# Performance work log

Measured on AMD Instinct MI355X. Metric: run time of the kernel, lower is better.

The kernel has to match this reference:

```python
import jax, jax.numpy as jnp
import numpy as np

B, N, D_IN, D, H_HEADS, DH, M_LAND, ITERS, NCLS = 2, 16384, 1024, 512, 8, 64, 256, 6, 2


def layer_norm(x, g, b, eps=1e-5):
    mu = x.mean(-1, keepdims=True)
    var = ((x - mu) ** 2).mean(-1, keepdims=True)
    return (x - mu) * jax.lax.rsqrt(var + eps) * g + b


def pinv_iter(x, iters):
    # Moore-Penrose pseudo-inverse via Newton-Schulz style iteration (lucidrains nystrom-attention)
    col = jnp.abs(x).sum(-1)
    row = jnp.abs(x).sum(-2)
    z = jnp.swapaxes(x, -1, -2) / (jnp.max(col) * jnp.max(row))
    I = jnp.eye(x.shape[-1], dtype=x.dtype)
    for _ in range(iters):
        xz = x @ z
        z = 0.25 * z @ (13.0 * I - xz @ (15.0 * I - xz @ (7.0 * I - xz)))
    return z


def depthwise_conv(x, w, pad_h, pad_w):
    # x: [B,C,H,W], w: [C,1,kh,kw], groups=C
    return jax.lax.conv_general_dilated(
        x, w, (1, 1), ((pad_h, pad_h), (pad_w, pad_w)),
        dimension_numbers=('NCHW', 'OIHW', 'NCHW'), feature_group_count=x.shape[1])


def nystrom_attention(x, w_qkv, w_out, b_out, res_w):
    b, n, _ = x.shape
    pad = (-n) % M_LAND
    xp = jnp.pad(x, ((0, 0), (pad, 0), (0, 0)))  # pad at front
    npad = n + pad
    qkv = xp @ w_qkv                              # [b, npad, 3D]
    q, k, v = jnp.split(qkv, 3, axis=-1)
    split_heads = lambda t: t.reshape(b, npad, H_HEADS, DH).transpose(0, 2, 1, 3)
    q = split_heads(q) * (DH ** -0.5)
    k = split_heads(k)
    v = split_heads(v)
    l = npad // M_LAND
    # landmarks: mean over contiguous groups '(m l) d -> m d'
    ql = q.reshape(b, H_HEADS, M_LAND, l, DH).mean(3)
    kl = k.reshape(b, H_HEADS, M_LAND, l, DH).mean(3)
    sim1 = jnp.einsum('bhnd,bhmd->bhnm', q, kl)   # [b,h,npad,m]
    sim2 = jnp.einsum('bhid,bhjd->bhij', ql, kl)  # [b,h,m,m]
    sim3 = jnp.einsum('bhmd,bhnd->bhmn', ql, k)   # [b,h,m,npad]
    a1 = jax.nn.softmax(sim1, -1)
    a2 = jax.nn.softmax(sim2, -1)
    a3 = jax.nn.softmax(sim3, -1)
    a2inv = pinv_iter(a2, ITERS)
    out = (a1 @ a2inv) @ (a3 @ v)                 # [b,h,npad,dh]
    # residual depthwise conv over sequence dim, kernel (33,1), per head
    out = out + depthwise_conv(v, res_w, 16, 0)
    out = out.transpose(0, 2, 1, 3).reshape(b, npad, D)
    out = out @ w_out + b_out                     # dropout is identity in eval
    return out[:, -n:]


def ppeg(x, Hs, Ws, w7, b7, w5, b5, w3, b3):
    Bx, _, C = x.shape
    cls_tok, feat = x[:, :1], x[:, 1:]
    f = feat.transpose(0, 2, 1).reshape(Bx, C, Hs, Ws)
    y = (f
         + depthwise_conv(f, w7, 3, 3) + b7[None, :, None, None]
         + depthwise_conv(f, w5, 2, 2) + b5[None, :, None, None]
         + depthwise_conv(f, w3, 1, 1) + b3[None, :, None, None])
    y = y.reshape(Bx, C, Hs * Ws).transpose(0, 2, 1)
    return jnp.concatenate([cls_tok, y], axis=1)


def _forward(x, w_feat, b_feat, cls_token, ln1_g, ln1_b, qkv1, out1_w, out1_b, res1_w,
             ppeg_w7, ppeg_b7, ppeg_w5, ppeg_b5, ppeg_w3, ppeg_b3,
             ln2_g, ln2_b, qkv2, out2_w, out2_b, res2_w, lnf_g, lnf_b, cls_w, cls_b):
    h = jax.nn.gelu(x @ w_feat + b_feat)          # feature embed (dropout off)
    n = h.shape[1]
    side = int(np.ceil(np.sqrt(n)))
    add = side * side - n
    h = jnp.concatenate([h, h[:, :add]], axis=1)  # pad bag to square
    cls = jnp.broadcast_to(cls_token, (h.shape[0], 1, D))
    h = jnp.concatenate([cls, h], axis=1)
    h = h + nystrom_attention(layer_norm(h, ln1_g, ln1_b), qkv1, out1_w, out1_b, res1_w)
    h = ppeg(h, side, side, ppeg_w7, ppeg_b7, ppeg_w5, ppeg_b5, ppeg_w3, ppeg_b3)
    h = h + nystrom_attention(layer_norm(h, ln2_g, ln2_b), qkv2, out2_w, out2_b, res2_w)
    feat0 = layer_norm(h, lnf_g, lnf_b)[:, 0]
    return feat0 @ cls_w + cls_b                  # logits [B, n_classes]


def setup_inputs() -> dict:
    key = jax.random.key(0)
    ks = jax.random.split(key, 16)
    s = jnp.float32(0.02)
    return {
        'x': jax.random.normal(ks[0], (B, N, D_IN), jnp.float32),
        'w_feat': jax.random.normal(ks[1], (D_IN, D), jnp.float32) * s,
        'b_feat': jnp.zeros((D,), jnp.float32),
        'cls_token': jax.random.normal(ks[2], (1, 1, D), jnp.float32) * jnp.float32(1e-6),
        'ln1_g': jnp.ones((D,), jnp.float32), 'ln1_b': jnp.zeros((D,), jnp.float32),
        'qkv1': jax.random.normal(ks[3], (D, 3 * D), jnp.float32) * s,
        'out1_w': jax.random.normal(ks[4], (D, D), jnp.float32) * s,
        'out1_b': jnp.zeros((D,), jnp.float32),
        'res1_w': jax.random.normal(ks[5], (H_HEADS, 1, 33, 1), jnp.float32) * s,
        'ppeg_w7': jax.random.normal(ks[6], (D, 1, 7, 7), jnp.float32) * s,
        'ppeg_b7': jnp.zeros((D,), jnp.float32),
        'ppeg_w5': jax.random.normal(ks[7], (D, 1, 5, 5), jnp.float32) * s,
        'ppeg_b5': jnp.zeros((D,), jnp.float32),
        'ppeg_w3': jax.random.normal(ks[8], (D, 1, 3, 3), jnp.float32) * s,
        'ppeg_b3': jnp.zeros((D,), jnp.float32),
        'ln2_g': jnp.ones((D,), jnp.float32), 'ln2_b': jnp.zeros((D,), jnp.float32),
        'qkv2': jax.random.normal(ks[9], (D, 3 * D), jnp.float32) * s,
        'out2_w': jax.random.normal(ks[10], (D, D), jnp.float32) * s,
        'out2_b': jnp.zeros((D,), jnp.float32),
        'res2_w': jax.random.normal(ks[11], (H_HEADS, 1, 33, 1), jnp.float32) * s,
        'lnf_g': jnp.ones((D,), jnp.float32), 'lnf_b': jnp.zeros((D,), jnp.float32),
        'cls_w': jax.random.normal(ks[12], (D, NCLS), jnp.float32) * s,
        'cls_b': jnp.zeros((NCLS,), jnp.float32),
    }


def reference(x, w_feat, b_feat, cls_token, ln1_g, ln1_b, qkv1, out1_w, out1_b, res1_w,
              ppeg_w7, ppeg_b7, ppeg_w5, ppeg_b5, ppeg_w3, ppeg_b3,
              ln2_g, ln2_b, qkv2, out2_w, out2_b, res2_w, lnf_g, lnf_b, cls_w, cls_b):
    return _forward(x, w_feat, b_feat, cls_token, ln1_g, ln1_b, qkv1, out1_w, out1_b, res1_w,
                    ppeg_w7, ppeg_b7, ppeg_w5, ppeg_b5, ppeg_w3, ppeg_b3,
                    ln2_g, ln2_b, qkv2, out2_w, out2_b, res2_w, lnf_g, lnf_b, cls_w, cls_b)
```

## Files before the change

### kernel.cpp

```cpp
#include <hip/hip_runtime.h>
#include <cstdint>
#include <cstddef>

#define BB 2
#define TT 16385
#define NPAD 16640
#define DD 512
#define HH 8
#define DHH 64
#define MLAND 256
#define PADF 255
#define A3KC 26
#define A3CH 640

typedef __attribute__((ext_vector_type(8))) _Float16 f16x8;
typedef __attribute__((ext_vector_type(4))) float f32x4;

__device__ __forceinline__ float gelu_f(float v) {
  float c = 0.7978845608028654f * (v + 0.044715f * v * v * v);
  return 0.5f * v * (1.0f + tanhf(c));
}

__device__ __forceinline__ unsigned short f16_1(float a) {
  _Float16 h = (_Float16)a;
  return __builtin_bit_cast(unsigned short, h);
}
__device__ __forceinline__ float f16f(unsigned u) {
  return (float)__builtin_bit_cast(_Float16, (unsigned short)(u & 0xffffu));
}
__device__ __forceinline__ unsigned pk_f16(float a, float b) {
  return (unsigned)f16_1(a) | ((unsigned)f16_1(b) << 16);
}
__device__ __forceinline__ void split2h(float a, float b, unsigned& hi, unsigned& lo) {
  _Float16 ah = (_Float16)a, bh = (_Float16)b;
  hi = (unsigned)__builtin_bit_cast(unsigned short, ah) |
       ((unsigned)__builtin_bit_cast(unsigned short, bh) << 16);
  lo = pk_f16(a - (float)ah, b - (float)bh);
}
__device__ __forceinline__ void store4h(float4 v, unsigned short* dh,
                                        unsigned short* dl) {
  unsigned h0, l0, h1, l1;
  split2h(v.x, v.y, h0, l0);
  split2h(v.z, v.w, h1, l1);
  *(uint2*)dh = make_uint2(h0, h1);
  *(uint2*)dl = make_uint2(l0, l1);
}

__device__ __forceinline__ void gload16(const unsigned short* g, short* l) {
  __builtin_amdgcn_global_load_lds(
      (const __attribute__((address_space(1))) void*)g,
      (__attribute__((address_space(3))) void*)l, 16, 0, 0);
}

__global__ void k_set_cls(float* __restrict__ h, const float* __restrict__ cls) {
  h[(size_t)blockIdx.x * TT * DD + threadIdx.x] = cls[threadIdx.x];
}
__global__ void k_copy_cls(float* __restrict__ dst, const float* __restrict__ src) {
  size_t o = (size_t)blockIdx.x * TT * DD + threadIdx.x;
  dst[o] = src[o];
}

__global__ __launch_bounds__(256) void k_cvt_wt(
    const float* __restrict__ W, unsigned short* __restrict__ Wth, int K, int N) {
  __shared__ float tile[32][33];
  int kb = blockIdx.x * 32, nb = blockIdx.y * 32;
  int t = threadIdx.x;
  int tr = t >> 3, tc4 = (t & 7) * 4;
  float4 v = *(const float4*)(W + (size_t)(kb + tr) * N + nb + tc4);
  tile[tr][tc4 + 0] = v.x;
  tile[tr][tc4 + 1] = v.y;
  tile[tr][tc4 + 2] = v.z;
  tile[tr][tc4 + 3] = v.w;
  __syncthreads();
  int n = nb + tr;
  ushort4 hs;
  hs.x = f16_1(tile[tc4 + 0][tr]);
  hs.y = f16_1(tile[tc4 + 1][tr]);
  hs.z = f16_1(tile[tc4 + 2][tr]);
  hs.w = f16_1(tile[tc4 + 3][tr]);
  *(ushort4*)(Wth + (size_t)n * K + kb + tc4) = hs;
}

template <int MODE>
__global__ __launch_bounds__(512) void k_gemm_mfma(
    const float* __restrict__ A, const unsigned short* __restrict__ Aph,
    const unsigned short* __restrict__ Apl, const unsigned short* __restrict__ Wth,
    const float* __restrict__ bias, void* __restrict__ Cv, int M, int K, int N,
    int lda) {
  __shared__ short Ash[128][44];
  __shared__ short Asl[128][44];
  __shared__ short Bsh[256][44];
  const int t = threadIdx.x;
  int nRow = gridDim.x, nCol = gridDim.y;
  int lin = blockIdx.x + blockIdx.y * nRow;
  int chunk = 8 * nCol;
  int group = lin / chunk;
  int rem = lin - group * chunk;
  int gbase = group * 8;
  int Geff = nRow - gbase;
  if (Geff > 8) Geff = 8;
  const int rb = (gbase + rem % Geff) * 128;
  const int cb = (rem / Geff) * 256;
  const float* Ab = A;
  float* Cf = (float*)Cv;
  unsigned short* Ch = (unsigned short*)Cv;
  if (MODE == 2) {
    int b = blockIdx.z;
    Ab = A + (size_t)b * NPAD * DD + (size_t)PADF * DD;
    Cf = (float*)Cv + (size_t)b * TT * DD;
  }
  const int lane = t & 63, wv = t >> 6;
  const int wr = wv >> 2, wc = wv & 3;
  const int fr = lane & 15, kg = lane >> 4;
  const int srow = t >> 2, skh = (t & 3) * 8;
  const int brow = t >> 1, bkh = (t & 1) * 16;

  f32x4 acc[4][4];
  f32x4 zero4 = {0.f, 0.f, 0.f, 0.f};
#pragma unroll
  for (int i = 0; i < 4; ++i)
#pragma unroll
    for (int j = 0; j < 4; ++j) acc[i][j] = zero4;

  for (int k0 = 0; k0 < K; k0 += 32) {
    __syncthreads();
    if (MODE == 1) {
      const unsigned short* ph = Aph + (size_t)(rb + srow) * lda + k0 + skh;
      const unsigned short* pl = Apl + (size_t)(rb + srow) * lda + k0 + skh;
      *(uint4*)&Ash[srow][skh] = *(const uint4*)ph;
      *(uint4*)&Asl[srow][skh] = *(const uint4*)pl;
    } else {
      int grow = rb + srow;
      float4 f0 = {0, 0, 0, 0}, f1 = {0, 0, 0, 0};
      if (grow < M) {
        const float* p = Ab + (size_t)grow * lda + k0 + skh;
        f0 = *(const float4*)p;
        f1 = *(const float4*)(p + 4);
      }
      unsigned h0, h1, h2, h3, l0, l1, l2, l3;
      split2h(f0.x, f0.y, h0, l0);
      split2h(f0.z, f0.w, h1, l1);
      split2h(f1.x, f1.y, h2, l2);
      split2h(f1.z, f1.w, h3, l3);
      *(uint4*)&Ash[srow][skh] = make_uint4(h0, h1, h2, h3);
      *(uint4*)&Asl[srow][skh] = make_uint4(l0, l1, l2, l3);
    }
    {
      const unsigned short* ph = Wth + (size_t)(cb + brow) * K + k0 + bkh;
      *(uint4*)&Bsh[brow][bkh] = *(const uint4*)ph;
      *(uint4*)&Bsh[brow][bkh + 8] = *(const uint4*)(ph + 8);
    }
    __syncthreads();
    f16x8 ah[4], al[4];
#pragma unroll
    for (int mf = 0; mf < 4; ++mf) {
      ah[mf] = *(const f16x8*)&Ash[wr * 64 + mf * 16 + fr][kg * 8];
      al[mf] = *(const f16x8*)&Asl[wr * 64 + mf * 16 + fr][kg * 8];
    }
#pragma unroll
    for (int nf = 0; nf < 4; ++nf) {
      f16x8 bhf = *(const f16x8*)&Bsh[wc * 64 + nf * 16 + fr][kg * 8];
#pragma unroll
      for (int mf = 0; mf < 4; ++mf) {
        acc[mf][nf] =
            __builtin_amdgcn_mfma_f32_16x16x32_f16(ah[mf], bhf, acc[mf][nf], 0, 0, 0);
        acc[mf][nf] =
            __builtin_amdgcn_mfma_f32_16x16x32_f16(al[mf], bhf, acc[mf][nf], 0, 0, 0);
      }
    }
  }
#pragma unroll
  for (int mf = 0; mf < 4; ++mf) {
#pragma unroll
    for (int r = 0; r < 4; ++r) {
      int row = rb + wr * 64 + mf * 16 + kg * 4 + r;
      if (MODE == 2 && row >= M) continue;
      size_t orow = (MODE == 0) ? (size_t)(row + (row >> 14) + 1) : (size_t)row;
#pragma unroll
      for (int nf = 0; nf < 4; ++nf) {
        int col = cb + wc * 64 + nf * 16 + fr;
        float v = acc[mf][nf][r];
        if (MODE == 0) {
          Cf[orow * DD + col] = gelu_f(v + bias[col]);
        } else if (MODE == 1) {
          Ch[orow * (size_t)N + col] = f16_1(v);
        } else {
          float old = Cf[orow * DD + col];
          Cf[orow * DD + col] = old + v + bias[col];
        }
      }
    }
  }
}

__global__ __launch_bounds__(512) void k_gemm_qkv8(
    const unsigned short* __restrict__ Aph, const unsigned short* __restrict__ Apl,
    const unsigned short* __restrict__ Wth, unsigned short* __restrict__ Ch) {
  __shared__ __align__(16) short Ah[2][128][32];
  __shared__ __align__(16) short Al[2][128][32];
  __shared__ __align__(16) short Bs[2][256][32];
  const int t = threadIdx.x;
  int nRow = gridDim.x, nCol = gridDim.y;
  int lin = blockIdx.x + blockIdx.y * nRow;
  int chunk = 8 * nCol;
  int group = lin / chunk;
  int rem = lin - group * chunk;
  int gbase = group * 8;
  int Geff = nRow - gbase;
  if (Geff > 8) Geff = 8;
  const int rb = (gbase + rem % Geff) * 128;
  const int cb = (rem / Geff) * 256;
  const int lane = t & 63, wv = t >> 6;
  const int wr = wv >> 2, wc = wv & 3;
  const int fr = lane & 15, kg = lane >> 4;
  const int lr4 = lane >> 2;
  const int ss = (lane & 3) ^ (lr4 & 3);

  f32x4 acc[4][4];
  f32x4 zero4 = {0.f, 0.f, 0.f, 0.f};
#pragma unroll
  for (int i = 0; i < 4; ++i)
#pragma unroll
    for (int j = 0; j < 4; ++j) acc[i][j] = zero4;

  auto STAGE = [&](int kt, int bf) {
    const int k0 = kt * 32;
    {
      int lr = wv * 16;
      gload16(Aph + (size_t)(rb + lr + lr4) * DD + k0 + ss * 8, &Ah[bf][lr][0]);
      gload16(Apl + (size_t)(rb + lr + lr4) * DD + k0 + ss * 8, &Al[bf][lr][0]);
    }
#pragma unroll
    for (int j = 0; j < 2; ++j) {
      int lr = wv * 32 + j * 16;
      gload16(Wth + (size_t)(cb + lr + lr4) * DD + k0 + ss * 8, &Bs[bf][lr][0]);
    }
  };

  STAGE(0, 0);
  STAGE(1, 1);
  const int sl = ((kg ^ (fr & 3))) * 8;
  for (int kt = 0; kt < 16; ++kt) {
    if (kt < 15) {
      asm volatile("s_waitcnt vmcnt(4)" ::: "memory");
    } else {
      asm volatile("s_waitcnt vmcnt(0)" ::: "memory");
    }
    __builtin_amdgcn_sched_barrier(0);
    __builtin_amdgcn_s_barrier();
    const int bf = kt & 1;
    f16x8 ah[4], al[4];
#pragma unroll
    for (int mf = 0; mf < 4; ++mf) {
      ah[mf] = *(const f16x8*)&Ah[bf][wr * 64 + mf * 16 + fr][sl];
      al[mf] = *(const f16x8*)&Al[bf][wr * 64 + mf * 16 + fr][sl];
    }
#pragma unroll
    for (int nf = 0; nf < 4; ++nf) {
      f16x8 bhf = *(const f16x8*)&Bs[bf][wc * 64 + nf * 16 + fr][sl];
#pragma unroll
      for (int mf = 0; mf < 4; ++mf) {
        acc[mf][nf] =
            __builtin_amdgcn_mfma_f32_16x16x32_f16(ah[mf], bhf, acc[mf][nf], 0, 0, 0);
        acc[mf][nf] =
            __builtin_amdgcn_mfma_f32_16x16x32_f16(al[mf], bhf, acc[mf][nf], 0, 0, 0);
      }
    }
    __builtin_amdgcn_s_barrier();
    if (kt + 2 < 16) STAGE(kt + 2, bf);
  }
#pragma unroll
  for (int mf = 0; mf < 4; ++mf) {
#pragma unroll
    for (int r = 0; r < 4; ++r) {
      int row = rb + wr * 64 + mf * 16 + kg * 4 + r;
#pragma unroll
      for (int nf = 0; nf < 4; ++nf) {
        int col = cb + wc * 64 + nf * 16 + fr;
        Ch[(size_t)row * 1536 + col] = f16_1(acc[mf][nf][r]);
      }
    }
  }
}

__global__ __launch_bounds__(256) void k_ln_pad(
    unsigned short* __restrict__ xph, unsigned short* __restrict__ xpl,
    const float* __restrict__ h, const float* __restrict__ gam,
    const float* __restrict__ bet) {
  int w = threadIdx.x >> 6, lane = threadIdx.x & 63;
  int row = blockIdx.x * 4 + w;
  if (row >= BB * TT) return;
  int b = row / TT, i = row - b * TT;
  const float* src = h + (size_t)row * DD;
  float4 x0 = *(const float4*)(src + lane * 4);
  float4 x1 = *(const float4*)(src + 256 + lane * 4);
  float s = x0.x + x0.y + x0.z + x0.w + x1.x + x1.y + x1.z + x1.w;
  for (int o = 32; o; o >>= 1) s += __shfl_xor(s, o);
  float mu = s * (1.f / 512.f);
  float q = (x0.x - mu) * (x0.x - mu) + (x0.y - mu) * (x0.y - mu) +
            (x0.z - mu) * (x0.z - mu) + (x0.w - mu) * (x0.w - mu) +
            (x1.x - mu) * (x1.x - mu) + (x1.y - mu) * (x1.y - mu) +
            (x1.z - mu) * (x1.z - mu) + (x1.w - mu) * (x1.w - mu);
  for (int o = 32; o; o >>= 1) q += __shfl_xor(q, o);
  float rs = rsqrtf(q * (1.f / 512.f) + 1e-5f);
  float4 g0 = *(const float4*)(gam + lane * 4);
  float4 g1 = *(const float4*)(gam + 256 + lane * 4);
  float4 b0 = *(const float4*)(bet + lane * 4);
  float4 b1 = *(const float4*)(bet + 256 + lane * 4);
  float4 o0, o1;
  o0.x = (x0.x - mu) * rs * g0.x + b0.x;
  o0.y = (x0.y - mu) * rs * g0.y + b0.y;
  o0.z = (x0.z - mu) * rs * g0.z + b0.z;
  o0.w = (x0.w - mu) * rs * g0.w + b0.w;
  o1.x = (x1.x - mu) * rs * g1.x + b1.x;
  o1.y = (x1.y - mu) * rs * g1.y + b1.y;
  o1.z = (x1.z - mu) * rs * g1.z + b1.z;
  o1.w = (x1.w - mu) * rs * g1.w + b1.w;
  size_t ro = ((size_t)b * NPAD + PADF + i) * DD;
  store4h(o0, xph + ro + lane * 4, xpl + ro + lane * 4);
  store4h(o1, xph + ro + 256 + lane * 4, xpl + ro + 256 + lane * 4);
}

__global__ void k_zero_pad(unsigned short* __restrict__ xph,
                           unsigned short* __restrict__ xpl) {
  int r = blockIdx.x;
  int b = r / PADF, j = r - b * PADF;
  size_t ro = ((size_t)b * NPAD + j) * DD;
  ((unsigned*)(xph + ro))[threadIdx.x] = 0u;
  ((unsigned*)(xpl + ro))[threadIdx.x] = 0u;
}

__global__ __launch_bounds__(256) void k_landmarks(
    float* __restrict__ ql, float* __restrict__ kl,
    const unsigned short* __restrict__ qkv) {
  int t = threadIdx.x;
  int mi = t >> 6, d = t & 63;
  int blk = blockIdx.x;
  int bh = blk >> 6, mg = blk & 63;
  int b = bh >> 3, h = bh & 7;
  int m = mg * 4 + mi;
  const unsigned short* base = qkv + (size_t)b * NPAD * 1536 + h * 64 + d;
  float sq = 0.f, sk = 0.f;
  int t0 = m * 65;
  for (int j = 0; j < 65; ++j) {
    const unsigned short* p = base + (size_t)(t0 + j) * 1536;
    sq += f16f(p[0]);
    sk += f16f(p[512]);
  }
  ql[((size_t)bh * 256 + m) * 64 + d] = sq * (0.125f / 65.f);
  kl[((size_t)bh * 256 + m) * 64 + d] = sk * (1.f / 65.f);
}

__global__ __launch_bounds__(256) void k_sim2(
    float* __restrict__ sim, const float* __restrict__ ql, const float* __restrict__ kl) {
  __shared__ __align__(16) float Aq[64][68];
  __shared__ __align__(16) float Bk[64][68];
  int t = threadIdx.x;
  int tj = blockIdx.x, ti = blockIdx.y, bh = blockIdx.z;
  int r = t >> 2, cc = (t & 3) * 16;
  const float* ap = ql + ((size_t)bh * 256 + ti * 64 + r) * 64 + cc;
  const float* bp = kl + ((size_t)bh * 256 + tj * 64 + r) * 64 + cc;
#pragma unroll
  for (int i = 0; i < 16; i += 4) {
    *(float4*)&Aq[r][cc + i] = *(const float4*)(ap + i);
    *(float4*)&Bk[r][cc + i] = *(const float4*)(bp + i);
  }
  __syncthreads();
  int tx = t & 15, ty = t >> 4;
  float acc[4][4];
#pragma unroll
  for (int i = 0; i < 4; ++i)
#pragma unroll
    for (int j = 0; j < 4; ++j) acc[i][j] = 0.f;
  for (int d = 0; d < 64; d += 4) {
    float4 a4[4], b4[4];
#pragma unroll
    for (int ii = 0; ii < 4; ++ii) a4[ii] = *(float4*)&Aq[ty * 4 + ii][d];
#pragma unroll
    for (int jj = 0; jj < 4; ++jj) b4[jj] = *(float4*)&Bk[tx * 4 + jj][d];
#pragma unroll
    for (int ii = 0; ii < 4; ++ii)
#pragma unroll
      for (int jj = 0; jj < 4; ++jj)
        acc[ii][jj] += a4[ii].x * b4[jj].x + a4[ii].y * b4[jj].y + a4[ii].z * b4[jj].z +
                       a4[ii].w * b4[jj].w;
  }
#pragma unroll
  for (int ii = 0; ii < 4; ++ii)
#pragma unroll
    for (int jj = 0; jj < 4; ++jj)
      sim[((size_t)bh * 256 + ti * 64 + ty * 4 + ii) * 256 + tj * 64 + tx * 4 + jj] =
          acc[ii][jj];
}

__global__ __launch_bounds__(256) void k_softmax256(float* __restrict__ a) {
  int w = threadIdx.x >> 6, lane = threadIdx.x & 63;
  size_t row = (size_t)blockIdx.x * 4 + w;
  float* p = a + row * 256 + lane * 4;
  float4 v = *(float4*)p;
  float m = fmaxf(fmaxf(v.x, v.y), fmaxf(v.z, v.w));
  for (int o = 32; o; o >>= 1) m = fmaxf(m, __shfl_xor(m, o));
  v.x = expf(v.x - m); v.y = expf(v.y - m);
  v.z = expf(v.z - m); v.w = expf(v.w - m);
  float s = v.x + v.y + v.z + v.w;
  for (int o = 32; o; o >>= 1) s += __shfl_xor(s, o);
  float inv = 1.f / s;
  v.x *= inv; v.y *= inv; v.z *= inv; v.w *= inv;
  *(float4*)p = v;
}

__global__ void k_pinv_sums(float* __restrict__ red, const float* __restrict__ a2) {
  int bh = blockIdx.x, t = threadIdx.x;
  const float* Ab = a2 + (size_t)bh * 65536;
  float s = 0.f;
  for (int i = 0; i < 256; ++i) s += fabsf(Ab[(size_t)i * 256 + t]);
  red[bh * 256 + t] = s;
  float c = 0.f;
  const float* rp = Ab + (size_t)t * 256;
  for (int j = 0; j < 256; j += 4) {
    float4 v = *(const float4*)(rp + j);
    c += fabsf(v.x) + fabsf(v.y) + fabsf(v.z) + fabsf(v.w);
  }
  red[4096 + bh * 256 + t] = c;
}

__global__ void k_pinv_scale(float* __restrict__ red) {
  __shared__ float sm[8];
  int t = threadIdx.x;
  float m1 = 0.f, m2 = 0.f;
  for (int k = t; k < 4096; k += 256) {
    m1 = fmaxf(m1, red[k]);
    m2 = fmaxf(m2, red[4096 + k]);
  }
  for (int o = 32; o; o >>= 1) {
    m1 = fmaxf(m1, __shfl_xor(m1, o));
    m2 = fmaxf(m2, __shfl_xor(m2, o));
  }
  int w = t >> 6;
  if ((t & 63) == 0) { sm[w] = m1; sm[4 + w] = m2; }
  __syncthreads();
  if (t == 0) {
    float a = fmaxf(fmaxf(sm[0], sm[1]), fmaxf(sm[2], sm[3]));
    float b = fmaxf(fmaxf(sm[4], sm[5]), fmaxf(sm[6], sm[7]));
    red[8192] = 1.0f / (a * b);
  }
}

__global__ void k_zinit(float* __restrict__ z, const float* __restrict__ a2,
                        const float* __restrict__ red) {
  float s = red[8192];
  int i = blockIdx.x, bh = blockIdx.y, j = threadIdx.x;
  z[((size_t)bh * 256 + i) * 256 + j] = a2[((size_t)bh * 256 + j) * 256 + i] * s;
}

__device__ __forceinline__ void bmm_core(
    short (*Ash)[136], short (*Asl)[136], short (*Bsh)[136], short (*Bsl)[136],
    const float* __restrict__ Ab, const float* __restrict__ Bb, int i0, int j0, int N,
    int t, f32x4 (&acc)[4]) {
  const int lane = t & 63, w = t >> 6;
  const int fr = lane & 15, kg = lane >> 4;
  const int ar = t >> 2, akseg = (t & 3) * 32;
  for (int k0 = 0; k0 < 256; k0 += 128) {
    __syncthreads();
    {
      const float* p = Ab + (size_t)(i0 + ar) * 256 + k0 + akseg;
#pragma unroll
      for (int q = 0; q < 4; ++q) {
        float4 f0 = *(const float4*)(p + q * 8);
        float4 f1 = *(const float4*)(p + q * 8 + 4);
        unsigned h0, h1, h2, h3, l0, l1, l2, l3;
        split2h(f0.x, f0.y, h0, l0);
        split2h(f0.z, f0.w, h1, l1);
        split2h(f1.x, f1.y, h2, l2);
        split2h(f1.z, f1.w, h3, l3);
        *(uint4*)&Ash[ar][akseg + q * 8] = make_uint4(h0, h1, h2, h3);
        *(uint4*)&Asl[ar][akseg + q * 8] = make_uint4(l0, l1, l2, l3);
      }
    }
    {
#pragma unroll
      for (int pass = 0; pass < 8; ++pass) {
        int kr = pass * 16 + (t >> 4);
        int jseg = (t & 15) * 4;
        const float* p = Bb + (size_t)(k0 + kr) * N + j0 + jseg;
        float4 f = *(const float4*)p;
        float fv[4] = {f.x, f.y, f.z, f.w};
#pragma unroll
        for (int c = 0; c < 4; ++c) {
          _Float16 hh = (_Float16)fv[c];
          float lo = fv[c] - (float)hh;
          Bsh[jseg + c][kr] = (short)__builtin_bit_cast(unsigned short, hh);
          Bsl[jseg + c][kr] = (short)f16_1(lo);
        }
      }
    }
    __syncthreads();
#pragma unroll
    for (int kw = 0; kw < 4; ++kw) {
      f16x8 bhf = *(const f16x8*)&Bsh[w * 16 + fr][kw * 32 + kg * 8];
      f16x8 blf = *(const f16x8*)&Bsl[w * 16 + fr][kw * 32 + kg * 8];
#pragma unroll
      for (int mf = 0; mf < 4; ++mf) {
        f16x8 ah = *(const f16x8*)&Ash[mf * 16 + fr][kw * 32 + kg * 8];
        f16x8 al = *(const f16x8*)&Asl[mf * 16 + fr][kw * 32 + kg * 8];
        acc[mf] = __builtin_amdgcn_mfma_f32_16x16x32_f16(ah, bhf, acc[mf], 0, 0, 0);
        acc[mf] = __builtin_amdgcn_mfma_f32_16x16x32_f16(al, bhf, acc[mf], 0, 0, 0);
        acc[mf] = __builtin_amdgcn_mfma_f32_16x16x32_f16(ah, blf, acc[mf], 0, 0, 0);
      }
    }
  }
}

__global__ __launch_bounds__(256) void k_bmm_poly(
    const float* __restrict__ A, const float* __restrict__ Bm,
    const float* __restrict__ E, float* __restrict__ C, float a1, float d1, float e1,
    int N) {
  __shared__ short Ash[64][136];
  __shared__ short Asl[64][136];
  __shared__ short Bsh[64][136];
  __shared__ short Bsl[64][136];
  const int t = threadIdx.x;
  const int bh = blockIdx.z;
  const int i0 = blockIdx.y * 64, j0 = blockIdx.x * 64;
  const int lane = t & 63, w = t >> 6;
  const int fr = lane & 15, kg = lane >> 4;
  f32x4 acc[4];
  f32x4 zero4 = {0.f, 0.f, 0.f, 0.f};
#pragma unroll
  for (int i = 0; i < 4; ++i) acc[i] = zero4;
  bmm_core(Ash, Asl, Bsh, Bsl, A + (size_t)bh * 65536, Bm + (size_t)bh * 256 * N, i0,
           j0, N, t, acc);
  int j = j0 + w * 16 + fr;
#pragma unroll
  for (int mf = 0; mf < 4; ++mf) {
#pragma unroll
    for (int rr = 0; rr < 4; ++rr) {
      int i = i0 + mf * 16 + kg * 4 + rr;
      float v = acc[mf][rr];
      size_t off = (size_t)bh * 256 * N + (size_t)i * N + j;
      float out = a1 * v + ((i == j) ? d1 : 0.f);
      if (E) out += e1 * E[off];
      C[off] = out;
    }
  }
}

__global__ __launch_bounds__(256) void k_bmm_dual(
    const float* __restrict__ A0, const float* __restrict__ A1,
    const float* __restrict__ Bm, float* __restrict__ C0, float* __restrict__ C1,
    float s) {
  __shared__ short Ash[64][136];
  __shared__ short Asl[64][136];
  __shared__ short Bsh[64][136];
  __shared__ short Bsl[64][136];
  const int t = threadIdx.x;
  const int z = blockIdx.z;
  const int bh = z & 15;
  const int sel = z >> 4;
  const float* A = sel ? A1 : A0;
  float* C = sel ? C1 : C0;
  const int i0 = blockIdx.y * 64, j0 = blockIdx.x * 64;
  const int lane = t & 63, w = t >> 6;
  const int fr = lane & 15, kg = lane >> 4;
  f32x4 acc[4];
  f32x4 zero4 = {0.f, 0.f, 0.f, 0.f};
#pragma unroll
  for (int i = 0; i < 4; ++i) acc[i] = zero4;
  bmm_core(Ash, Asl, Bsh, Bsl, A + (size_t)bh * 65536, Bm + (size_t)bh * 65536, i0, j0,
           256, t, acc);
  int j = j0 + w * 16 + fr;
#pragma unroll
  for (int mf = 0; mf < 4; ++mf) {
#pragma unroll
    for (int rr = 0; rr < 4; ++rr) {
      int i = i0 + mf * 16 + kg * 4 + rr;
      size_t off = (size_t)bh * 65536 + (size_t)i * 256 + j;
      C[off] = s * acc[mf][rr];
    }
  }
}

__global__ __launch_bounds__(256, 2) void k_a3v_mfma(
    float* __restrict__ pacc, float* __restrict__ pL,
    const float* __restrict__ ql, const unsigned short* __restrict__ qkv) {
  __shared__ short Ks[64][72];
  __shared__ short Vt[64][72];
  __shared__ short Ps[4][64][72];
  const int t = threadIdx.x;
  const int bh = blockIdx.x;
  const int kc = blockIdx.y;
  const int b = bh >> 3, h = bh & 7;
  const int lane = t & 63, w = t >> 6;
  const int fr = lane & 15, kg = lane >> 4;

  f16x8 qf[4][2];
#pragma unroll
  for (int nf = 0; nf < 4; ++nf) {
    const float* qp = ql + ((size_t)bh * 256 + w * 64 + nf * 16 + fr) * 64 + kg * 8;
#pragma unroll
    for (int kw = 0; kw < 2; ++kw) {
      float4 a = *(const float4*)(qp + kw * 32);
      float4 c = *(const float4*)(qp + kw * 32 + 4);
      uint4 uu = make_uint4(pk_f16(a.x, a.y), pk_f16(a.z, a.w), pk_f16(c.x, c.y),
                            pk_f16(c.z, c.w));
      qf[nf][kw] = *(f16x8*)&uu;
    }
  }
  f32x4 oacc[4][4];
  f32x4 zero4 = {0.f, 0.f, 0.f, 0.f};
#pragma unroll
  for (int i = 0; i < 4; ++i)
#pragma unroll
    for (int j = 0; j < 4; ++j) oacc[i][j] = zero4;
  float Lp[4] = {0.f, 0.f, 0.f, 0.f};

  const int skey = t >> 2, sd = (t & 3) * 16;
  const unsigned short* kbase = qkv + (size_t)b * NPAD * 1536 + 512 + h * 64 + sd;

  for (int it = 0; it < A3CH / 64; ++it) {
    int nt = kc * A3CH + it * 64;
    __syncthreads();
    {
      const unsigned short* kp = kbase + (size_t)(nt + skey) * 1536;
      *(uint4*)&Ks[skey][sd] = *(const uint4*)kp;
      *(uint4*)&Ks[skey][sd + 8] = *(const uint4*)(kp + 8);
      const unsigned short* vp = kp + 512;
      uint4 v01 = *(const uint4*)vp;
      uint4 v23 = *(const uint4*)(vp + 8);
      Vt[sd + 0][skey] = (short)v01.x;
      Vt[sd + 1][skey] = (short)(v01.x >> 16);
      Vt[sd + 2][skey] = (short)v01.y;
      Vt[sd + 3][skey] = (short)(v01.y >> 16);
      Vt[sd + 4][skey] = (short)v01.z;
      Vt[sd + 5][skey] = (short)(v01.z >> 16);
      Vt[sd + 6][skey] = (short)v01.w;
      Vt[sd + 7][skey] = (short)(v01.w >> 16);
      Vt[sd + 8][skey] = (short)v23.x;
      Vt[sd + 9][skey] = (short)(v23.x >> 16);
      Vt[sd + 10][skey] = (short)v23.y;
      Vt[sd + 11][skey] = (short)(v23.y >> 16);
      Vt[sd + 12][skey] = (short)v23.z;
      Vt[sd + 13][skey] = (short)(v23.z >> 16);
      Vt[sd + 14][skey] = (short)v23.w;
      Vt[sd + 15][skey] = (short)(v23.w >> 16);
    }
    __syncthreads();
    f32x4 sacc[4][4];
#pragma unroll
    for (int i = 0; i < 4; ++i)
#pragma unroll
      for (int j = 0; j < 4; ++j) sacc[i][j] = zero4;
#pragma unroll
    for (int kw = 0; kw < 2; ++kw) {
      f16x8 kf[4];
#pragma unroll
      for (int mf = 0; mf < 4; ++mf)
        kf[mf] = *(const f16x8*)&Ks[mf * 16 + fr][kw * 32 + kg * 8];
#pragma unroll
      for (int mf = 0; mf < 4; ++mf)
#pragma unroll
        for (int nf = 0; nf < 4; ++nf)
          sacc[mf][nf] = __builtin_amdgcn_mfma_f32_16x16x32_f16(kf[mf], qf[nf][kw],
                                                                sacc[mf][nf], 0, 0, 0);
    }
#pragma unroll
    for (int mf = 0; mf < 4; ++mf)
#pragma unroll
      for (int nf = 0; nf < 4; ++nf) {
        f32x4 s = sacc[mf][nf];
        float p0 = __expf(s[0]);
        float p1 = __expf(s[1]);
        float p2 = __expf(s[2]);
        float p3 = __expf(s[3]);
        Lp[nf] += (p0 + p1) + (p2 + p3);
        uint2 pw = make_uint2(pk_f16(p0, p1), pk_f16(p2, p3));
        *(uint2*)&Ps[w][nf * 16 + fr][mf * 16 + kg * 4] = pw;
      }
    __syncthreads();
#pragma unroll
    for (int kw = 0; kw < 2; ++kw) {
      f16x8 vf[4], pf[4];
#pragma unroll
      for (int mf = 0; mf < 4; ++mf)
        vf[mf] = *(const f16x8*)&Vt[mf * 16 + fr][kw * 32 + kg * 8];
#pragma unroll
      for (int nf = 0; nf < 4; ++nf)
        pf[nf] = *(const f16x8*)&Ps[w][nf * 16 + fr][kw * 32 + kg * 8];
#pragma unroll
      for (int mf = 0; mf < 4; ++mf)
#pragma unroll
        for (int nf = 0; nf < 4; ++nf)
          oacc[mf][nf] = __builtin_amdgcn_mfma_f32_16x16x32_f16(vf[mf], pf[nf],
                                                                oacc[mf][nf], 0, 0, 0);
    }
  }
  size_t obase = ((size_t)kc * 16 + bh) * 256;
#pragma unroll
  for (int mf = 0; mf < 4; ++mf)
#pragma unroll
    for (int nf = 0; nf < 4; ++nf) {
      int lm = w * 64 + nf * 16 + fr;
      *(f32x4*)(pacc + (obase + lm) * 64 + mf * 16 + kg * 4) = oacc[mf][nf];
    }
#pragma unroll
  for (int nf = 0; nf < 4; ++nf) {
    Lp[nf] += __shfl_xor(Lp[nf], 16);
    Lp[nf] += __shfl_xor(Lp[nf], 32);
  }
  if (lane < 16) {
#pragma unroll
    for (int nf = 0; nf < 4; ++nf)
      pL[obase + w * 64 + nf * 16 + lane] = Lp[nf];
  }
}

__global__ __launch_bounds__(64) void k_a3v_red(
    float* __restrict__ bv, const float* __restrict__ pacc,
    const float* __restrict__ pL) {
  int row = blockIdx.x;
  int d = threadIdx.x;
  float A = 0.f, L = 0.f;
#pragma unroll
  for (int c = 0; c < A3KC; ++c) {
    size_t pr = (size_t)c * 4096 + row;
    A += pacc[pr * 64 + d];
    L += pL[pr];
  }
  bv[(size_t)row * 64 + d] = A / L;
}

__global__ __launch_bounds__(256, 2) void k_att1(
    float* __restrict__ attout, const unsigned short* __restrict__ qkv,
    const float* __restrict__ kl, const float* __restrict__ w2) {
  __shared__ short KLs[64][72];
  __shared__ short W2t[64][72];
  __shared__ short Ps[4][64][72];
  const int t = threadIdx.x;
  const int tile = blockIdx.x, bh = blockIdx.y;
  const int b = bh >> 3, h = bh & 7;
  const int lane = t & 63, w = t >> 6;
  const int fr = lane & 15, kg = lane >> 4;
  const int n0 = tile * 256;

  f16x8 qf[4][2];
#pragma unroll
  for (int nf = 0; nf < 4; ++nf) {
    const unsigned short* qp =
        qkv + ((size_t)b * NPAD + n0 + w * 64 + nf * 16 + fr) * 1536 + h * 64 + kg * 8;
    qf[nf][0] = *(const f16x8*)qp;
    qf[nf][1] = *(const f16x8*)(qp + 32);
  }
  f32x4 oacc[4][4];
  f32x4 zero4 = {0.f, 0.f, 0.f, 0.f};
#pragma unroll
  for (int i = 0; i < 4; ++i)
#pragma unroll
    for (int j = 0; j < 4; ++j) oacc[i][j] = zero4;
  float Lp[4] = {0.f, 0.f, 0.f, 0.f};

  const int sr = t >> 2, sc = (t & 3) * 16;
  for (int cb = 0; cb < 4; ++cb) {
    __syncthreads();
    {
      const float* kp = kl + ((size_t)bh * 256 + cb * 64 + sr) * 64 + sc;
      float4 k0 = *(const float4*)kp;
      float4 k1 = *(const float4*)(kp + 4);
      float4 k2 = *(const float4*)(kp + 8);
      float4 k3 = *(const float4*)(kp + 12);
      *(uint4*)&KLs[sr][sc] =
          make_uint4(pk_f16(k0.x * 0.125f, k0.y * 0.125f),
                     pk_f16(k0.z * 0.125f, k0.w * 0.125f),
                     pk_f16(k1.x * 0.125f, k1.y * 0.125f),
                     pk_f16(k1.z * 0.125f, k1.w * 0.125f));
      *(uint4*)&KLs[sr][sc + 8] =
          make_uint4(pk_f16(k2.x * 0.125f, k2.y * 0.125f),
                     pk_f16(k2.z * 0.125f, k2.w * 0.125f),
                     pk_f16(k3.x * 0.125f, k3.y * 0.125f),
                     pk_f16(k3.z * 0.125f, k3.w * 0.125f));
      const float* wp = w2 + ((size_t)bh * 256 + cb * 64 + sr) * 64 + sc;
      float4 v0 = *(const float4*)wp;
      float4 v1 = *(const float4*)(wp + 4);
      float4 v2 = *(const float4*)(wp + 8);
      float4 v3 = *(const float4*)(wp + 12);
      W2t[sc + 0][sr] = (short)f16_1(v0.x);
      W2t[sc + 1][sr] = (short)f16_1(v0.y);
      W2t[sc + 2][sr] = (short)f16_1(v0.z);
      W2t[sc + 3][sr] = (short)f16_1(v0.w);
      W2t[sc + 4][sr] = (short)f16_1(v1.x);
      W2t[sc + 5][sr] = (short)f16_1(v1.y);
      W2t[sc + 6][sr] = (short)f16_1(v1.z);
      W2t[sc + 7][sr] = (short)f16_1(v1.w);
      W2t[sc + 8][sr] = (short)f16_1(v2.x);
      W2t[sc + 9][sr] = (short)f16_1(v2.y);
      W2t[sc + 10][sr] = (short)f16_1(v2.z);
      W2t[sc + 11][sr] = (short)f16_1(v2.w);
      W2t[sc + 12][sr] = (short)f16_1(v3.x);
      W2t[sc + 13][sr] = (short)f16_1(v3.y);
      W2t[sc + 14][sr] = (short)f16_1(v3.z);
      W2t[sc + 15][sr] = (short)f16_1(v3.w);
    }
    __syncthreads();
    f32x4 sacc[4][4];
#pragma unroll
    for (int i = 0; i < 4; ++i)
#pragma unroll
      for (int j = 0; j < 4; ++j) sacc[i][j] = zero4;
#pragma unroll
    for (int kw = 0; kw < 2; ++kw) {
      f16x8 kf[4];
#pragma unroll
      for (int mf = 0; mf < 4; ++mf)
        kf[mf] = *(const f16x8*)&KLs[mf * 16 + fr][kw * 32 + kg * 8];
#pragma unroll
      for (int mf = 0; mf < 4; ++mf)
#pragma unroll
        for (int nf = 0; nf < 4; ++nf)
          sacc[mf][nf] = __builtin_amdgcn_mfma_f32_16x16x32_f16(kf[mf], qf[nf][kw],
                                                                sacc[mf][nf], 0, 0, 0);
    }
#pragma unroll
    for (int mf = 0; mf < 4; ++mf)
#pragma unroll
      for (int nf = 0; nf < 4; ++nf) {
        f32x4 s = sacc[mf][nf];
        float p0 = __expf(s[0]);
        float p1 = __expf(s[1]);
        float p2 = __expf(s[2]);
        float p3 = __expf(s[3]);
        Lp[nf] += (p0 + p1) + (p2 + p3);
        uint2 pw = make_uint2(pk_f16(p0, p1), pk_f16(p2, p3));
        *(uint2*)&Ps[w][nf * 16 + fr][mf * 16 + kg * 4] = pw;
      }
    __syncthreads();
#pragma unroll
    for (int kw = 0; kw < 2; ++kw) {
      f16x8 vf[4], pf[4];
#pragma unroll
      for (int mf = 0; mf < 4; ++mf)
        vf[mf] = *(const f16x8*)&W2t[mf * 16 + fr][kw * 32 + kg * 8];
#pragma unroll
      for (int nf = 0; nf < 4; ++nf)
        pf[nf] = *(const f16x8*)&Ps[w][nf * 16 + fr][kw * 32 + kg * 8];
#pragma unroll
      for (int mf = 0; mf < 4; ++mf)
#pragma unroll
        for (int nf = 0; nf < 4; ++nf)
          oacc[mf][nf] = __builtin_amdgcn_mfma_f32_16x16x32_f16(vf[mf], pf[nf],
                                                                oacc[mf][nf], 0, 0, 0);
    }
  }
#pragma unroll
  for (int nf = 0; nf < 4; ++nf) {
    Lp[nf] += __shfl_xor(Lp[nf], 16);
    Lp[nf] += __shfl_xor(Lp[nf], 32);
  }
#pragma unroll
  for (int nf = 0; nf < 4; ++nf) {
    float inv = 1.0f / Lp[nf];
    int tok = n0 + w * 64 + nf * 16 + fr;
#pragma unroll
    for (int mf = 0; mf < 4; ++mf) {
      f32x4 o = oacc[mf][nf];
      o[0] *= inv; o[1] *= inv; o[2] *= inv; o[3] *= inv;
      *(f32x4*)(attout + ((size_t)b * NPAD + tok) * DD + h * 64 + mf * 16 + kg * 4) = o;
    }
  }
}

__global__ __launch_bounds__(256) void k_convres(
    float* __restrict__ attout, const unsigned short* __restrict__ qkv,
    const float* __restrict__ resw) {
  __shared__ float vS[96][68];
  __shared__ float w33[33];
  int t = threadIdx.x;
  int tb = blockIdx.x, bh = blockIdx.y;
  int b = bh >> 3, h = bh & 7;
  int n0 = tb * 64;
  if (t < 33) w33[t] = resw[h * 33 + t];
  int sc = (t & 3) * 16;
#pragma unroll
  for (int pass = 0; pass < 2; ++pass) {
    int r = (t >> 2) + pass * 64;
    if (r < 96) {
      int seq = n0 - 16 + r;
      if (seq >= 0 && seq < NPAD) {
        const unsigned short* p =
            qkv + ((size_t)b * NPAD + seq) * 1536 + 1024 + h * 64 + sc;
        uint4 u0 = *(const uint4*)p;
        uint4 u1 = *(const uint4*)(p + 8);
        float4 f0 = make_float4(f16f(u0.x), f16f(u0.x >> 16), f16f(u0.y),
                                f16f(u0.y >> 16));
        float4 f1 = make_float4(f16f(u0.z), f16f(u0.z >> 16), f16f(u0.w),
                                f16f(u0.w >> 16));
        float4 f2 = make_float4(f16f(u1.x), f16f(u1.x >> 16), f16f(u1.y),
                                f16f(u1.y >> 16));
        float4 f3 = make_float4(f16f(u1.z), f16f(u1.z >> 16), f16f(u1.w),
                                f16f(u1.w >> 16));
        *(float4*)&vS[r][sc + 0] = f0;
        *(float4*)&vS[r][sc + 4] = f1;
        *(float4*)&vS[r][sc + 8] = f2;
        *(float4*)&vS[r][sc + 12] = f3;
      } else {
        float4 z = make_float4(0.f, 0.f, 0.f, 0.f);
        *(float4*)&vS[r][sc + 0] = z;
        *(float4*)&vS[r][sc + 4] = z;
        *(float4*)&vS[r][sc + 8] = z;
        *(float4*)&vS[r][sc + 12] = z;
      }
    }
  }
  __syncthreads();
  int tg = t >> 5;
  int d2 = (t & 31) * 2;
  float ax[8], ay[8];
#pragma unroll
  for (int j = 0; j < 8; ++j) { ax[j] = 0.f; ay[j] = 0.f; }
#pragma unroll
  for (int rr = 0; rr < 40; ++rr) {
    float2 v = *(float2*)&vS[tg * 8 + rr][d2];
#pragma unroll
    for (int j = 0; j < 8; ++j) {
      int k = rr - j;
      if (k >= 0 && k < 33) {
        ax[j] += w33[k] * v.x;
        ay[j] += w33[k] * v.y;
      }
    }
  }
#pragma unroll
  for (int j = 0; j < 8; ++j) {
    float* dst = attout + ((size_t)b * NPAD + n0 + tg * 8 + j) * DD + h * 64 + d2;
    float2 o = *(float2*)dst;
    o.x += ax[j];
    o.y += ay[j];
    *(float2*)dst = o;
  }
}

__global__ __launch_bounds__(128) void k_ppeg(
    float* __restrict__ hB, const float* __restrict__ hA,
    const float* __restrict__ w7, const float* __restrict__ b7,
    const float* __restrict__ w5, const float* __restrict__ b5,
    const float* __restrict__ w3, const float* __restrict__ b3) {
  __shared__ float cw[49][128];
  int t = threadIdx.x;
  int i = blockIdx.x >> 2;
  int j0 = (blockIdx.x & 3) * 32;
  int cg = blockIdx.y, b = blockIdx.z;
  int c = cg * 128 + t;
#pragma unroll
  for (int k = 0; k < 49; ++k) cw[k][t] = w7[c * 49 + k];
#pragma unroll
  for (int di = 0; di < 5; ++di)
#pragma unroll
    for (int dj = 0; dj < 5; ++dj)
      cw[(di + 1) * 7 + dj + 1][t] += w5[c * 25 + di * 5 + dj];
#pragma unroll
  for (int di = 0; di < 3; ++di)
#pragma unroll
    for (int dj = 0; dj < 3; ++dj)
      cw[(di + 2) * 7 + dj + 2][t] += w3[c * 9 + di * 3 + dj];
  cw[24][t] += 1.0f;
  float bias = b7[c] + b5[c] + b3[c];
  const float* base = hA + (size_t)b * TT * DD + DD + c;
  float* obase = hB + (size_t)b * TT * DD + DD + c;
  float acc[32];
#pragma unroll
  for (int j = 0; j < 32; ++j) acc[j] = bias;
  for (int di = 0; di < 7; ++di) {
    int ii = i + di - 3;
    if ((unsigned)ii >= 128u) continue;
    float win[38];
#pragma unroll
    for (int w = 0; w < 38; ++w) {
      int col = j0 - 3 + w;
      win[w] = ((unsigned)col < 128u) ? base[(size_t)(ii * 128 + col) * DD] : 0.f;
    }
#pragma unroll
    for (int dj = 0; dj < 7; ++dj) {
      float wv = cw[di * 7 + dj][t];
#pragma unroll
      for (int j = 0; j < 32; ++j) acc[j] += win[j + dj] * wv;
    }
  }
#pragma unroll
  for (int j = 0; j < 32; ++j) obase[(size_t)(i * 128 + j0 + j) * DD] = acc[j];
}

__global__ __launch_bounds__(512) void k_final(
    float* __restrict__ out, const float* __restrict__ h,
    const float* __restrict__ g, const float* __restrict__ be,
    const float* __restrict__ cw, const float* __restrict__ cbias) {
  __shared__ float sm[16];
  int t = threadIdx.x;
  for (int b = 0; b < 2; ++b) {
    const float* row = h + (size_t)b * TT * DD;
    float x = row[t];
    float s = x;
    for (int o = 32; o; o >>= 1) s += __shfl_xor(s, o);
    if ((t & 63) == 0) sm[t >> 6] = s;
    __syncthreads();
    float mu = 0.f;
    for (int i = 0; i < 8; ++i) mu += sm[i];
    mu *= (1.f / 512.f);
    __syncthreads();
    float d = x - mu;
    s = d * d;
    for (int o = 32; o; o >>= 1) s += __shfl_xor(s, o);
    if ((t & 63) == 0) sm[t >> 6] = s;
    __syncthreads();
    float var = 0.f;
    for (int i = 0; i < 8; ++i) var += sm[i];
    var *= (1.f / 512.f);
    float rs = rsqrtf(var + 1e-5f);
    __syncthreads();
    float f = d * rs * g[t] + be[t];
    float p0 = f * cw[2 * t], p1 = f * cw[2 * t + 1];
    for (int o = 32; o; o >>= 1) {
      p0 += __shfl_xor(p0, o);
      p1 += __shfl_xor(p1, o);
    }
    if ((t & 63) == 0) {
      sm[t >> 6] = p0;
      sm[8 + (t >> 6)] = p1;
    }
    __syncthreads();
    if (t == 0) {
      float q0 = 0.f, q1 = 0.f;
      for (int i = 0; i < 8; ++i) {
        q0 += sm[i];
        q1 += sm[8 + i];
      }
      out[b * 2 + 0] = q0 + cbias[0];
      out[b * 2 + 1] = q1 + cbias[1];
    }
    __syncthreads();
  }
}

static void run_attn(float* h, const float* lng, const float* lnb,
                     const float* wqkv, const float* wout, const float* bout,
                     const float* resw, float* xp, unsigned short* qkvh, float* ql,
                     float* kl, float* a2, float* z0, float* z1, float* xz, float* xz2,
                     float* yB, float* yC, float* bv, float* w2, float* red,
                     float* Sbuf, unsigned short* wth, hipStream_t stream) {
  unsigned short* xph = (unsigned short*)xp;
  unsigned short* xpl = xph + (size_t)BB * NPAD * DD;
  k_zero_pad<<<BB * PADF, 256, 0, stream>>>(xph, xpl);
  k_ln_pad<<<(BB * TT + 3) / 4, 256, 0, stream>>>(xph, xpl, h, lng, lnb);
  k_cvt_wt<<<dim3(DD / 32, 1536 / 32), 256, 0, stream>>>(wqkv, wth, DD, 1536);
  k_gemm_qkv8<<<dim3(BB * NPAD / 128, 1536 / 256), 512, 0, stream>>>(xph, xpl, wth,
                                                                     qkvh);
  k_landmarks<<<1024, 256, 0, stream>>>(ql, kl, qkvh);
  float* pacc = Sbuf;
  float* pL = Sbuf + (size_t)A3KC * 4096 * 64;
  k_a3v_mfma<<<dim3(16, A3KC), 256, 0, stream>>>(pacc, pL, ql, qkvh);
  k_a3v_red<<<4096, 64, 0, stream>>>(bv, pacc, pL);
  k_sim2<<<dim3(4, 4, 16), 256, 0, stream>>>(a2, ql, kl);
  k_softmax256<<<1024, 256, 0, stream>>>(a2);
  k_pinv_sums<<<16, 256, 0, stream>>>(red, a2);
  k_pinv_scale<<<1, 256, 0, stream>>>(red);
  k_zinit<<<dim3(256, 16), 256, 0, stream>>>(z0, a2, red);
  float* zc = z0;
  float* zn = z1;
  float* P = xz;
  float* Pn = xz2;
  k_bmm_poly<<<dim3(4, 4, 16), 256, 0, stream>>>(a2, zc, nullptr, P, 1.f, 0.f, 0.f, 256);
  for (int it = 0; it < 6; ++it) {
    k_bmm_poly<<<dim3(4, 4, 16), 256, 0, stream>>>(P, P, P, yB, 1.f, 15.f, -7.f, 256);
    k_bmm_poly<<<dim3(4, 4, 16), 256, 0, stream>>>(P, yB, nullptr, yC, -1.f, 13.f, 0.f, 256);
    k_bmm_dual<<<dim3(4, 4, 32), 256, 0, stream>>>(zc, P, yC, zn, Pn, 0.25f);
    float* tmp = zc; zc = zn; zn = tmp;
    tmp = P; P = Pn; Pn = tmp;
  }
  k_bmm_poly<<<dim3(1, 4, 16), 256, 0, stream>>>(zc, bv, nullptr, w2, 1.f, 0.f, 0.f, 64);
  k_att1<<<dim3(NPAD / 256, 16), 256, 0, stream>>>(xp, qkvh, kl, w2);
  k_convres<<<dim3(NPAD / 64, 16), 256, 0, stream>>>(xp, qkvh, resw);
  k_cvt_wt<<<dim3(DD / 32, DD / 32), 256, 0, stream>>>(wout, wth, DD, DD);
  k_gemm_mfma<2><<<dim3(129, 2, BB), 512, 0, stream>>>(xp, nullptr, nullptr, wth, bout,
                                                       h, TT, DD, DD, DD);
}

extern "C" void kernel_launch(void* const* d_in, const int* in_sizes, int n_in,
                              void* d_out, int out_size, void* d_ws, size_t ws_size,
                              hipStream_t stream) {
  const float* x        = (const float*)d_in[0];
  const float* w_feat   = (const float*)d_in[1];
  const float* b_feat   = (const float*)d_in[2];
  const float* cls_tok  = (const float*)d_in[3];
  const float* ln1_g    = (const float*)d_in[4];
  const float* ln1_b    = (const float*)d_in[5];
  const float* qkv1     = (const float*)d_in[6];
  const float* out1_w   = (const float*)d_in[7];
  const float* out1_b   = (const float*)d_in[8];
  const float* res1_w   = (const float*)d_in[9];
  const float* ppeg_w7  = (const float*)d_in[10];
  const float* ppeg_b7  = (const float*)d_in[11];
  const float* ppeg_w5  = (const float*)d_in[12];
  const float* ppeg_b5  = (const float*)d_in[13];
  const float* ppeg_w3  = (const float*)d_in[14];
  const float* ppeg_b3  = (const float*)d_in[15];
  const float* ln2_g    = (const float*)d_in[16];
  const float* ln2_b    = (const float*)d_in[17];
  const float* qkv2     = (const float*)d_in[18];
  const float* out2_w   = (const float*)d_in[19];
  const float* out2_b   = (const float*)d_in[20];
  const float* res2_w   = (const float*)d_in[21];
  const float* lnf_g    = (const float*)d_in[22];
  const float* lnf_b    = (const float*)d_in[23];
  const float* cls_w    = (const float*)d_in[24];
  const float* cls_b    = (const float*)d_in[25];

  float* ws = (float*)d_ws;
  size_t off = 0;
  float* hA  = ws + off; off += (size_t)BB * TT * DD;
  float* hB  = ws + off; off += (size_t)BB * TT * DD;
  float* xp  = ws + off; off += (size_t)BB * NPAD * DD;
  float* qkvf = ws + off; off += (size_t)BB * NPAD * 3 * DD;
  unsigned short* qkvh = (unsigned short*)qkvf;
  float* ql  = ws + off; off += (size_t)BB * HH * 256 * 64;
  float* kl  = ws + off; off += (size_t)BB * HH * 256 * 64;
  float* a2  = ws + off; off += (size_t)16 * 65536;
  float* z0  = ws + off; off += (size_t)16 * 65536;
  float* z1  = ws + off; off += (size_t)16 * 65536;
  float* xz  = ws + off; off += (size_t)16 * 65536;
  float* xz2 = ws + off; off += (size_t)16 * 65536;
  float* yB  = ws + off; off += (size_t)16 * 65536;
  float* yC  = ws + off; off += (size_t)16 * 65536;
  float* bv  = ws + off; off += (size_t)BB * HH * 256 * 64;
  float* w2  = ws + off; off += (size_t)BB * HH * 256 * 64;
  float* red = ws + off; off += 8448;
  unsigned short* wth = (unsigned short*)(ws + off); off += 393216;

  k_set_cls<<<2, 512, 0, stream>>>(hA, cls_tok);
  k_cvt_wt<<<dim3(1024 / 32, DD / 32), 256, 0, stream>>>(w_feat, wth, 1024, DD);
  k_gemm_mfma<0><<<dim3(32768 / 128, DD / 256), 512, 0, stream>>>(
      x, nullptr, nullptr, wth, b_feat, hA, 32768, 1024, DD, 1024);
  run_attn(hA, ln1_g, ln1_b, qkv1, out1_w, out1_b, res1_w, xp, qkvh, ql, kl, a2, z0, z1,
           xz, xz2, yB, yC, bv, w2, red, hB, wth, stream);
  k_copy_cls<<<2, 512, 0, stream>>>(hB, hA);
  k_ppeg<<<dim3(512, 4, 2), 128, 0, stream>>>(hB, hA, ppeg_w7, ppeg_b7, ppeg_w5, ppeg_b5,
                                              ppeg_w3, ppeg_b3);
  run_attn(hB, ln2_g, ln2_b, qkv2, out2_w, out2_b, res2_w, xp, qkvh, ql, kl, a2, z0, z1,
           xz, xz2, yB, yC, bv, w2, red, hA, wth, stream);
  k_final<<<1, 512, 0, stream>>>((float*)d_out, hB, lnf_g, lnf_b, cls_w, cls_b);
}
```

Measured before the change: 1.540 ms.

## Store attention output in fp16 and use single-pass fp16 output projection GEMM

The attention kernel and conv residual now write and update the attention output as fp16 instead of fp32, halving that buffer's traffic. A new output-projection GEMM reads the fp16 activations directly and issues one MFMA per tile, where the old path split into hi/lo fp16 parts and issued two. It also adds the residual and bias in its epilogue. The cost is lower precision on attention outputs and on the conv residual accumulate, which may affect accuracy.

Result: faster. 1.451 ms (-5.8%).

```diff
diff --git a/kernel.cpp b/kernel.cpp
--- a/kernel.cpp
+++ b/kernel.cpp
@@ -278,6 +278,93 @@
       for (int nf = 0; nf < 4; ++nf) {
         int col = cb + wc * 64 + nf * 16 + fr;
         Ch[(size_t)row * 1536 + col] = f16_1(acc[mf][nf][r]);
+      }
+    }
+  }
+}
+
+__global__ __launch_bounds__(512) void k_gemm_proj(
+    const unsigned short* __restrict__ Af, const unsigned short* __restrict__ Wth,
+    float* __restrict__ Cb, const float* __restrict__ bias) {
+  __shared__ __align__(16) short Ah[2][128][32];
+  __shared__ __align__(16) short Bs[2][256][32];
+  const int t = threadIdx.x;
+  int nRow = gridDim.x, nCol = gridDim.y;
+  int lin = blockIdx.x + blockIdx.y * nRow;
+  int chunk = 8 * nCol;
+  int group = lin / chunk;
+  int rem = lin - group * chunk;
+  int gbase = group * 8;
+  int Geff = nRow - gbase;
+  if (Geff > 8) Geff = 8;
+  const int rb = (gbase + rem % Geff) * 128;
+  const int cb = (rem / Geff) * 256;
+  const int lane = t & 63, wv = t >> 6;
+  const int wr = wv >> 2, wc = wv & 3;
+  const int fr = lane & 15, kg = lane >> 4;
+  const int lr4 = lane >> 2;
+  const int ss = (lane & 3) ^ (lr4 & 3);
+  const size_t arow0 = (size_t)blockIdx.z * NPAD + PADF + rb;
+
+  f32x4 acc[4][4];
+  f32x4 zero4 = {0.f, 0.f, 0.f, 0.f};
+#pragma unroll
+  for (int i = 0; i < 4; ++i)
+#pragma unroll
+    for (int j = 0; j < 4; ++j) acc[i][j] = zero4;
+
+  auto STAGE = [&](int kt, int bf) {
+    const int k0 = kt * 32;
+    {
+      int lr = wv * 16;
+      gload16(Af + (arow0 + lr + lr4) * DD + k0 + ss * 8, &Ah[bf][lr][0]);
+    }
+#pragma unroll
+    for (int j = 0; j < 2; ++j) {
+      int lr = wv * 32 + j * 16;
+      gload16(Wth + (size_t)(cb + lr + lr4) * DD + k0 + ss * 8, &Bs[bf][lr][0]);
+    }
+  };
+
+  STAGE(0, 0);
+  STAGE(1, 1);
+  const int sl = ((kg ^ (fr & 3))) * 8;
+  for (int kt = 0; kt < 16; ++kt) {
+    if (kt < 15) {
+      asm volatile("s_waitcnt vmcnt(3)" ::: "memory");
+    } else {
+      asm volatile("s_waitcnt vmcnt(0)" ::: "memory");
+    }
+    __builtin_amdgcn_sched_barrier(0);
+    __builtin_amdgcn_s_barrier();
+    const int bf = kt & 1;
+    f16x8 ah[4];
+#pragma unroll
+    for (int mf = 0; mf < 4; ++mf)
+      ah[mf] = *(const f16x8*)&Ah[bf][wr * 64 + mf * 16 + fr][sl];
+#pragma unroll
+    for (int nf = 0; nf < 4; ++nf) {
+      f16x8 bhf = *(const f16x8*)&Bs[bf][wc * 64 + nf * 16 + fr][sl];
+#pragma unroll
+      for (int mf = 0; mf < 4; ++mf)
+        acc[mf][nf] =
+            __builtin_amdgcn_mfma_f32_16x16x32_f16(ah[mf], bhf, acc[mf][nf], 0, 0, 0);
+    }
+    __builtin_amdgcn_s_barrier();
+    if (kt + 2 < 16) STAGE(kt + 2, bf);
+  }
+  float* Cf = Cb + (size_t)blockIdx.z * TT * DD;
+#pragma unroll
+  for (int mf = 0; mf < 4; ++mf) {
+#pragma unroll
+    for (int r = 0; r < 4; ++r) {
+      int row = rb + wr * 64 + mf * 16 + kg * 4 + r;
+      if (row >= TT) continue;
+#pragma unroll
+      for (int nf = 0; nf < 4; ++nf) {
+        int col = cb + wc * 64 + nf * 16 + fr;
+        float old = Cf[(size_t)row * DD + col];
+        Cf[(size_t)row * DD + col] = old + acc[mf][nf][r] + bias[col];
       }
     }
   }
@@ -730,7 +817,7 @@
 }
 
 __global__ __launch_bounds__(256, 2) void k_att1(
-    float* __restrict__ attout, const unsigned short* __restrict__ qkv,
+    unsigned short* __restrict__ attf, const unsigned short* __restrict__ qkv,
     const float* __restrict__ kl, const float* __restrict__ w2) {
   __shared__ short KLs[64][72];
   __shared__ short W2t[64][72];
@@ -861,14 +948,18 @@
 #pragma unroll
     for (int mf = 0; mf < 4; ++mf) {
       f32x4 o = oacc[mf][nf];
-      o[0] *= inv; o[1] *= inv; o[2] *= inv; o[3] *= inv;
-      *(f32x4*)(attout + ((size_t)b * NPAD + tok) * DD + h * 64 + mf * 16 + kg * 4) = o;
+      ushort4 hs;
+      hs.x = f16_1(o[0] * inv);
+      hs.y = f16_1(o[1] * inv);
+      hs.z = f16_1(o[2] * inv);
+      hs.w = f16_1(o[3] * inv);
+      *(ushort4*)(attf + ((size_t)b * NPAD + tok) * DD + h * 64 + mf * 16 + kg * 4) = hs;
     }
   }
 }
 
 __global__ __launch_bounds__(256) void k_convres(
-    float* __restrict__ attout, const unsigned short* __restrict__ qkv,
+    unsigned short* __restrict__ attf, const unsigned short* __restrict__ qkv,
     const float* __restrict__ resw) {
   __shared__ float vS[96][68];
   __shared__ float w33[33];
@@ -929,11 +1020,11 @@
   }
 #pragma unroll
   for (int j = 0; j < 8; ++j) {
-    float* dst = attout + ((size_t)b * NPAD + n0 + tg * 8 + j) * DD + h * 64 + d2;
-    float2 o = *(float2*)dst;
-    o.x += ax[j];
-    o.y += ay[j];
-    *(float2*)dst = o;
+    size_t off = ((size_t)b * NPAD + n0 + tg * 8 + j) * DD + h * 64 + d2;
+    unsigned u = *(unsigned*)(attf + off);
+    float x0 = f16f(u) + ax[j];
+    float x1 = f16f(u >> 16) + ay[j];
+    *(unsigned*)(attf + off) = pk_f16(x0, x1);
   }
 }
 
@@ -1074,11 +1165,10 @@
     tmp = P; P = Pn; Pn = tmp;
   }
   k_bmm_poly<<<dim3(1, 4, 16), 256, 0, stream>>>(zc, bv, nullptr, w2, 1.f, 0.f, 0.f, 64);
-  k_att1<<<dim3(NPAD / 256, 16), 256, 0, stream>>>(xp, qkvh, kl, w2);
-  k_convres<<<dim3(NPAD / 64, 16), 256, 0, stream>>>(xp, qkvh, resw);
+  k_att1<<<dim3(NPAD / 256, 16), 256, 0, stream>>>(xph, qkvh, kl, w2);
+  k_convres<<<dim3(NPAD / 64, 16), 256, 0, stream>>>(xph, qkvh, resw);
   k_cvt_wt<<<dim3(DD / 32, DD / 32), 256, 0, stream>>>(wout, wth, DD, DD);
-  k_gemm_mfma<2><<<dim3(129, 2, BB), 512, 0, stream>>>(xp, nullptr, nullptr, wth, bout,
-                                                       h, TT, DD, DD, DD);
+  k_gemm_proj<<<dim3(129, 2, BB), 512, 0, stream>>>(xph, wth, h, bout);
 }
 
 extern "C" void kernel_launch(void* const* d_in, const int* in_sizes, int n_in,
```
